# Kernel tuning notes

Hardware: AMD Instinct MI355X
Metric: run time of the kernel (lower is better)

The kernel has to match this reference:

```python
import jax, jax.numpy as jnp
import numpy as np

EPS = 1e-5   # torch BatchNorm2d default eps
HEADS = 4


def conv1x1_bn(x, w, g, b, m, v):
    # 1x1 conv (no bias) == channel matmul, then inference-mode BatchNorm
    y = jnp.einsum('oc,bchw->bohw', w, x)
    s = g / jnp.sqrt(v + EPS)
    return y * s[None, :, None, None] + (b - m * s)[None, :, None, None]


def dwconv3x3_bn(x, w, g, b, m, v):
    # depthwise 3x3 conv, padding 1 (autopad), groups=C, then BatchNorm
    C = x.shape[1]
    y = jax.lax.conv_general_dilated(
        x, w, window_strides=(1, 1), padding=((1, 1), (1, 1)),
        dimension_numbers=('NCHW', 'OIHW', 'NCHW'), feature_group_count=C)
    s = g / jnp.sqrt(v + EPS)
    return y * s[None, :, None, None] + (b - m * s)[None, :, None, None]


def split_heads(x):
    b, c, h, w = x.shape
    hd = c // HEADS
    return x.reshape(b, HEADS, hd, h * w).transpose(0, 1, 3, 2)  # [b,heads,n,hd]


def merge_heads(x, h, w):
    b, heads, n, hd = x.shape
    return x.transpose(0, 1, 3, 2).reshape(b, heads * hd, h, w)


def setup_inputs() -> dict:
    key = jax.random.key(0)
    B, C, H, W = 4, 256, 48, 48
    ks = jax.random.split(key, 32)
    inp = {
        'q': jax.random.normal(ks[0], (B, C, H, W), jnp.float32),
        'k': jax.random.normal(ks[1], (B, C, H, W), jnp.float32),
        'v': jax.random.normal(ks[2], (B, C, H, W), jnp.float32),
    }
    i = 3
    for name in ['wq', 'wk', 'wv', 'proj']:
        inp[name + '_w'] = jax.random.normal(ks[i], (C, C), jnp.float32) * 0.02; i += 1
    inp['pe_w'] = jax.random.normal(ks[i], (C, 1, 3, 3), jnp.float32) * 0.1; i += 1
    for name in ['wq', 'wk', 'wv', 'pe', 'proj']:
        inp[name + '_g'] = jax.random.uniform(ks[i], (C,), jnp.float32, 0.5, 1.5); i += 1
        inp[name + '_b'] = jax.random.normal(ks[i], (C,), jnp.float32) * 0.1; i += 1
        inp[name + '_m'] = jax.random.normal(ks[i], (C,), jnp.float32) * 0.1; i += 1
        inp[name + '_v'] = jax.random.uniform(ks[i], (C,), jnp.float32, 0.5, 1.5); i += 1
    return inp


def reference(q, k, v,
              wq_w, wk_w, wv_w, proj_w, pe_w,
              wq_g, wq_b, wq_m, wq_v,
              wk_g, wk_b, wk_m, wk_v,
              wv_g, wv_b, wv_m, wv_v,
              pe_g, pe_b, pe_m, pe_v,
              proj_g, proj_b, proj_m, proj_v):
    H, W = q.shape[2], q.shape[3]
    qf = conv1x1_bn(q, wq_w, wq_g, wq_b, wq_m, wq_v)
    kf = conv1x1_bn(k, wk_w, wk_g, wk_b, wk_m, wk_v)
    vf = conv1x1_bn(v, wv_w, wv_g, wv_b, wv_m, wv_v)
    qh = split_heads(qf)  # [b,heads,n,hd]
    kh = split_heads(kf)
    vh = split_heads(vf)
    scale = qh.shape[-1] ** -0.5
    attn = jax.nn.softmax(jnp.einsum('bhnd,bhmd->bhnm', qh, kh) * scale, axis=-1)
    y = jnp.einsum('bhnm,bhmd->bhnd', attn, vh)
    y = merge_heads(y, H, W) + dwconv3x3_bn(merge_heads(qh, H, W), pe_w, pe_g, pe_b, pe_m, pe_v)
    return conv1x1_bn(y, proj_w, proj_g, proj_b, proj_m, proj_v)
```

## Files before the change

### kernel.cpp

```cpp
#include <hip/hip_runtime.h>
#include <math.h>

#define HEADS 4
#define HD    64
#define CCH   256
#define NB    4
#define HH    48
#define WW    48
#define NN    (HH*WW)
#define EPSBN 1e-5f
#define KSCL  0.18033688f
#define BCN   (NB*CCH*NN)
#define NSP   4

typedef unsigned short ushort_t;
typedef __attribute__((ext_vector_type(8))) short bfrag;
typedef __attribute__((ext_vector_type(4))) float f32x4;

#define MFMA __builtin_amdgcn_mfma_f32_16x16x32_bf16

static __device__ __forceinline__ ushort_t f2bf(float x) {
    unsigned int u = __float_as_uint(x);
    unsigned int r = (u + 0x7fffu + ((u >> 16) & 1u)) >> 16;
    return (ushort_t)r;
}
static __device__ __forceinline__ unsigned cvtpk(float lo, float hi) {
    unsigned r;
    asm("v_cvt_pk_bf16_f32 %0, %1, %2" : "=v"(r) : "v"(lo), "v"(hi));
    return r;
}
static __device__ __forceinline__ float bflo(unsigned u) { return __uint_as_float(u << 16); }
static __device__ __forceinline__ float bfhi(unsigned u) { return __uint_as_float(u & 0xffff0000u); }

static __device__ __forceinline__ void gload16(const void* g, void* l) {
    __builtin_amdgcn_global_load_lds(
        (const __attribute__((address_space(1))) void*)g,
        (__attribute__((address_space(3))) void*)l, 16, 0, 0);
}

struct PrepWP {
    const float* W[4];
    const float* G[4]; const float* Bb[4]; const float* Mm[4]; const float* Vv[4];
    const float* pew; const float* peg; const float* peb; const float* pem; const float* pev;
    ushort_t* W4; float* bias4; ushort_t* pw2; float* pbias; float* kmax2;
    const float* q; const float* k; const float* v; ushort_t* Xt;
};
__global__ __launch_bounds__(256)
void prep_kernel(PrepWP P)
{
    const int blk = blockIdx.x, tid = threadIdx.x;
    if (blk < 3456) {
        const int t  = blk / 1152;
        const int r  = blk % 1152;
        const int b  = r / 288;
        const int r2 = r % 288;
        const int n0 = (r2 >> 3) * 64;
        const int cb = (r2 & 7) * 32;
        const float* X = (t == 0) ? P.q : (t == 1) ? P.k : P.v;
        ushort_t* O = P.Xt + (size_t)t * BCN;
        const int lane = tid & 63;
        const int c0   = cb + (tid >> 6) * 8;
        const float* src = X + ((size_t)(b * CCH + c0) * NN + n0 + lane);
        float vv[8];
#pragma unroll
        for (int j = 0; j < 8; ++j) vv[j] = src[(size_t)j * NN];
        uint4 u;
        u.x = cvtpk(vv[0], vv[1]); u.y = cvtpk(vv[2], vv[3]);
        u.z = cvtpk(vv[4], vv[5]); u.w = cvtpk(vv[6], vv[7]);
        *(uint4*)&O[((size_t)b * NN + n0 + lane) * CCH + c0] = u;
        return;
    }
    const int wb = blk - 3456;
    if (wb == 128) {
        int c = tid;
        float s = P.peg[c] * rsqrtf(P.pev[c] + EPSBN);
        for (int tap = 0; tap < 9; ++tap)
            P.pw2[tap * CCH + c] = f2bf(P.pew[c * 9 + tap] * s);
        P.pbias[c] = P.peb[c] - P.pem[c] * s;
        if (tid < 16) P.kmax2[tid] = 0.f;
        return;
    }
    int g  = wb * 256 + tid;
    int cv = g >> 13;
    int o  = (g >> 5) & 255;
    int c8 = g & 31;
    float s  = P.G[cv][o] * rsqrtf(P.Vv[cv][o] + EPSBN);
    float s2 = (cv == 1) ? s * KSCL : s;
    const float* w = P.W[cv] + (size_t)o * CCH + c8 * 8;
    uint4 u;
    u.x = cvtpk(w[0]*s2, w[1]*s2); u.y = cvtpk(w[2]*s2, w[3]*s2);
    u.z = cvtpk(w[4]*s2, w[5]*s2); u.w = cvtpk(w[6]*s2, w[7]*s2);
    *(uint4*)&P.W4[((size_t)cv * CCH + o) * CCH + c8 * 8] = u;
    if (c8 == 0) {
        float bb = (P.Bb[cv][o] - P.Mm[cv][o] * s);
        P.bias4[cv * CCH + o] = (cv == 1) ? bb * KSCL : bb;
    }
}

template<int PROJ>
__global__ __launch_bounds__(256)
void conv_gemm(const ushort_t* __restrict__ T, const ushort_t* __restrict__ W4,
               const float* __restrict__ bias4,
               ushort_t* __restrict__ qnd, ushort_t* __restrict__ knd,
               ushort_t* __restrict__ vcn, float* __restrict__ outf,
               float* __restrict__ kmax2)
{
    __shared__ ushort_t Ts[64][264];
    __shared__ ushort_t Ws[64][264];
    const int nt = blockIdx.x, ot = blockIdx.y, z = blockIdx.z;
    const int which = PROJ ? 3 : (z >> 2);
    const int b = z & 3;
    const int tid = threadIdx.x;
    const int n0 = nt * 64, o0 = ot * 64;
    const ushort_t* Tsrc = T + (PROJ ? (size_t)0 : (size_t)which * BCN) + ((size_t)b * NN + n0) * CCH;
    const ushort_t* Wsrc = W4 + (size_t)which * CCH * CCH + (size_t)o0 * CCH;
    const float*    bias = bias4 + which * CCH;
#pragma unroll
    for (int i = 0; i < 8; ++i) {
        int idx = tid + i * 256;
        int r = idx >> 5, c16 = idx & 31;
        *(uint4*)&Ts[r][c16 * 8] = *(const uint4*)&Tsrc[(size_t)r * CCH + c16 * 8];
        *(uint4*)&Ws[r][c16 * 8] = *(const uint4*)&Wsrc[(size_t)r * CCH + c16 * 8];
    }
    __syncthreads();
    const int wv = tid >> 6, lane = tid & 63, lr = lane & 15, lg = lane >> 4;
    const int qn = (wv >> 1) * 32, qo = (wv & 1) * 32;
    f32x4 acc[2][2];
#pragma unroll
    for (int i = 0; i < 2; ++i)
#pragma unroll
        for (int j = 0; j < 2; ++j) acc[i][j] = (f32x4){0.f, 0.f, 0.f, 0.f};

    if (!PROJ && (z >> 2) < 2) {
#pragma unroll
        for (int k8 = 0; k8 < 8; ++k8) {
            const int kc = k8 * 32 + lg * 8;
            bfrag ta0 = *(const bfrag*)&Ts[qn + lr][kc];
            bfrag ta1 = *(const bfrag*)&Ts[qn + 16 + lr][kc];
            bfrag wa0 = *(const bfrag*)&Ws[qo + lr][kc];
            bfrag wa1 = *(const bfrag*)&Ws[qo + 16 + lr][kc];
            acc[0][0] = MFMA(ta0, wa0, acc[0][0], 0, 0, 0);
            acc[0][1] = MFMA(ta0, wa1, acc[0][1], 0, 0, 0);
            acc[1][0] = MFMA(ta1, wa0, acc[1][0], 0, 0, 0);
            acc[1][1] = MFMA(ta1, wa1, acc[1][1], 0, 0, 0);
        }
    } else {
#pragma unroll
        for (int k8 = 0; k8 < 8; ++k8) {
            const int kc = k8 * 32 + lg * 8;
            bfrag ta0 = *(const bfrag*)&Ts[qn + lr][kc];
            bfrag ta1 = *(const bfrag*)&Ts[qn + 16 + lr][kc];
            bfrag wa0 = *(const bfrag*)&Ws[qo + lr][kc];
            bfrag wa1 = *(const bfrag*)&Ws[qo + 16 + lr][kc];
            acc[0][0] = MFMA(wa0, ta0, acc[0][0], 0, 0, 0);
            acc[0][1] = MFMA(wa0, ta1, acc[0][1], 0, 0, 0);
            acc[1][0] = MFMA(wa1, ta0, acc[1][0], 0, 0, 0);
            acc[1][1] = MFMA(wa1, ta1, acc[1][1], 0, 0, 0);
        }
    }

    __syncthreads();
    if (!PROJ && which < 2) {
        ushort_t (*Ot)[72] = (ushort_t(*)[72])Ts;
        float bv[2] = { bias[o0 + qo + lr], bias[o0 + qo + 16 + lr] };
#pragma unroll
        for (int i = 0; i < 2; ++i)
#pragma unroll
            for (int j = 0; j < 2; ++j)
#pragma unroll
                for (int r = 0; r < 4; ++r)
                    Ot[qn + i * 16 + lg * 4 + r][qo + j * 16 + lr] = f2bf(acc[i][j][r] + bv[j]);
        __syncthreads();
        ushort_t* out = (which == 0) ? qnd : knd;
        for (int idx = tid; idx < 512; idx += 256) {
            int r = idx >> 3, sg = idx & 7;
            *(uint4*)&out[(((size_t)b * HEADS + ot) * NN + n0 + r) * HD + sg * 8] =
                *(const uint4*)&Ot[r][sg * 8];
        }
        if (which == 1 && tid < 64) {
            float s = 0.f;
#pragma unroll
            for (int j = 0; j < 8; ++j) {
                uint4 u = *(const uint4*)&Ot[tid][j * 8];
                s += bflo(u.x)*bflo(u.x) + bfhi(u.x)*bfhi(u.x);
                s += bflo(u.y)*bflo(u.y) + bfhi(u.y)*bfhi(u.y);
                s += bflo(u.z)*bflo(u.z) + bfhi(u.z)*bfhi(u.z);
                s += bflo(u.w)*bflo(u.w) + bfhi(u.w)*bfhi(u.w);
            }
            atomicMax((unsigned*)&kmax2[b * HEADS + ot], __float_as_uint(s));
        }
    } else if (!PROJ) {
        ushort_t (*Ot)[72] = (ushort_t(*)[72])Ts;
#pragma unroll
        for (int i = 0; i < 2; ++i)
#pragma unroll
            for (int r = 0; r < 4; ++r) {
                float bv = bias[o0 + qo + i * 16 + lg * 4 + r];
#pragma unroll
                for (int j = 0; j < 2; ++j)
                    Ot[qo + i * 16 + lg * 4 + r][qn + j * 16 + lr] = f2bf(acc[i][j][r] + bv);
            }
        __syncthreads();
        for (int idx = tid; idx < 512; idx += 256) {
            int r = idx >> 3, sg = idx & 7;
            *(uint4*)&vcn[((size_t)b * CCH + o0 + r) * NN + n0 + sg * 8] =
                *(const uint4*)&Ot[r][sg * 8];
        }
    } else {
        float (*Of)[68] = (float(*)[68])Ts;
#pragma unroll
        for (int i = 0; i < 2; ++i)
#pragma unroll
            for (int r = 0; r < 4; ++r) {
                float bv = bias[o0 + qo + i * 16 + lg * 4 + r];
#pragma unroll
                for (int j = 0; j < 2; ++j)
                    Of[qo + i * 16 + lg * 4 + r][qn + j * 16 + lr] = acc[i][j][r] + bv;
            }
        __syncthreads();
        for (int idx = tid; idx < 1024; idx += 256) {
            int r = idx >> 4, c4 = idx & 15;
            *(float4*)&outf[((size_t)b * CCH + o0 + r) * NN + n0 + c4 * 4] =
                *(const float4*)&Of[r][c4 * 4];
        }
    }
}

__global__ __launch_bounds__(256, 4)
void attn_kernel(const ushort_t* __restrict__ Qnd,
                 const ushort_t* __restrict__ Knd,
                 const ushort_t* __restrict__ Vcn,
                 const float* __restrict__ kmax2,
                 ushort_t* __restrict__ Op,
                 float* __restrict__ Larr)
{
    __shared__ __align__(16) char smem[32768];

    const int tid = threadIdx.x;
    const int lin0 = blockIdx.x + 18 * blockIdx.y + 288 * blockIdx.z;
    const int w    = (lin0 & 7) * 144 + (lin0 >> 3);
    const int qt = w % 18;
    const int bh = (w / 18) & 15;
    const int sp = w / 288;
    const int b = bh >> 2, h = bh & 3;
    const int lane = tid & 63, wv = tid >> 6;
    const int lr = lane & 15, lg = lane >> 4;
    const int lrow = lane >> 3, lslot = (lane & 7) ^ lrow;
    const int n0 = qt * 128;
    const size_t ndb = (size_t)(b * HEADS + h) * NN * HD;
    const size_t cnb = ((size_t)b * CCH + h * HD) * NN;

    const char* kgp = (const char*)(Knd + ndb) + (size_t)(sp * 576 + wv * 16 + lrow) * 128 + lslot * 16;
    const char* vgp = (const char*)(Vcn + cnb + sp * 576) + (size_t)(wv * 16 + lrow) * (NN * 2) + lslot * 16;
    char* kls = smem + wv * 2048;
    char* vls = smem + 16384 + wv * 2048;

#define STAGE_K(buf, t) do { \
    const char* kp_ = kgp + (size_t)(t) * 8192; \
    char* kd_ = kls + (buf) * 8192; \
    gload16(kp_,        kd_); \
    gload16(kp_ + 1024, kd_ + 1024); \
} while (0)
#define STAGE_V(buf, t) do { \
    const char* vp_ = vgp + (size_t)(t) * 128; \
    char* vd_ = vls + (buf) * 8192; \
    gload16(vp_,              vd_); \
    gload16(vp_ + 8 * (NN*2), vd_ + 1024); \
} while (0)

    bfrag qb[2][2];
    {
        const ushort_t* qbase = Qnd + ndb + (size_t)(n0 + wv * 32 + lr) * HD;
        qb[0][0] = *(const bfrag*)&qbase[lg * 8];
        qb[0][1] = *(const bfrag*)&qbase[32 + lg * 8];
        qb[1][0] = *(const bfrag*)&qbase[16 * HD + lg * 8];
        qb[1][1] = *(const bfrag*)&qbase[16 * HD + 32 + lg * 8];
    }
    float m0[2];
    {
        const float kmx = sqrtf(kmax2[bh]);
#pragma unroll
        for (int qc = 0; qc < 2; ++qc) {
            const unsigned* u0 = (const unsigned*)&qb[qc][0];
            const unsigned* u1 = (const unsigned*)&qb[qc][1];
            float s = 0.f;
#pragma unroll
            for (int j = 0; j < 4; ++j) {
                float a0 = bflo(u0[j]), a1 = bfhi(u0[j]);
                float b0 = bflo(u1[j]), b1 = bfhi(u1[j]);
                s += a0*a0 + a1*a1 + b0*b0 + b1*b1;
            }
            s += __shfl_xor(s, 16);
            s += __shfl_xor(s, 32);
            m0[qc] = sqrtf(s) * kmx + 0.5f;
        }
    }
    bfrag ones_f;
    {
        short ov = (lr == 0) ? (short)0x3F80 : (short)0;
#pragma unroll
        for (int j = 0; j < 8; ++j) ones_f[j] = ov;
    }

    f32x4 o[2][4], o4[2];
#pragma unroll
    for (int qc = 0; qc < 2; ++qc) {
        o4[qc] = (f32x4){0.f, 0.f, 0.f, 0.f};
#pragma unroll
        for (int db = 0; db < 4; ++db) o[qc][db] = (f32x4){0.f, 0.f, 0.f, 0.f};
    }

    const int sw0 = (lg ^ (lr & 7)) << 4;
    const int sw1 = ((4 + lg) ^ (lr & 7)) << 4;

    STAGE_K(0, 0);
    STAGE_V(0, 0);
    __syncthreads();

    for (int t = 0; t < 9; ++t) {
        const int cur = t & 1;
        if (t < 8) STAGE_K(cur ^ 1, t + 1);
        const char* Kb = smem + cur * 8192;
        const char* Vb = smem + 16384 + cur * 8192;
        char* Pw = smem + 16384 + (cur ^ 1) * 8192 + wv * 2048;

        uint2 pd[2][4];
#pragma unroll
        for (int kb = 0; kb < 4; ++kb) {
            const char* krow = Kb + (kb * 16 + lr) * 128;
            bfrag ka0 = *(const bfrag*)(krow + sw0);
            bfrag ka1 = *(const bfrag*)(krow + sw1);
            f32x4 z0 = (f32x4){-m0[0], -m0[0], -m0[0], -m0[0]};
            z0 = MFMA(ka0, qb[0][0], z0, 0, 0, 0);
            f32x4 s0 = MFMA(ka1, qb[0][1], z0, 0, 0, 0);
            f32x4 z1 = (f32x4){-m0[1], -m0[1], -m0[1], -m0[1]};
            z1 = MFMA(ka0, qb[1][0], z1, 0, 0, 0);
            f32x4 s1 = MFMA(ka1, qb[1][1], z1, 0, 0, 0);
            pd[0][kb].x = cvtpk(exp2f(s0[0]), exp2f(s0[1]));
            pd[0][kb].y = cvtpk(exp2f(s0[2]), exp2f(s0[3]));
            pd[1][kb].x = cvtpk(exp2f(s1[0]), exp2f(s1[1]));
            pd[1][kb].y = cvtpk(exp2f(s1[2]), exp2f(s1[3]));
        }

        bfrag pb[2][2];
#pragma unroll
        for (int qc = 0; qc < 2; ++qc) {
            char* prow = Pw + lr * 128;
#pragma unroll
            for (int kb = 0; kb < 4; ++kb) {
                int slot = (2 * kb + (lg >> 1)) ^ (lr & 7);
                *(uint2*)(prow + slot * 16 + (lg & 1) * 8) = pd[qc][kb];
            }
            pb[qc][0] = *(const bfrag*)(prow + sw0);
            pb[qc][1] = *(const bfrag*)(prow + sw1);
        }
        asm volatile("s_waitcnt lgkmcnt(0)" ::: "memory");
        if (t < 8) STAGE_V(cur ^ 1, t + 1);

#pragma unroll
        for (int db = 0; db < 4; ++db) {
            const char* vrow = Vb + (db * 16 + lr) * 128;
            bfrag va0 = *(const bfrag*)(vrow + sw0);
            bfrag va1 = *(const bfrag*)(vrow + sw1);
            o[0][db] = MFMA(va0, pb[0][0], o[0][db], 0, 0, 0);
            o[0][db] = MFMA(va1, pb[0][1], o[0][db], 0, 0, 0);
            o[1][db] = MFMA(va0, pb[1][0], o[1][db], 0, 0, 0);
            o[1][db] = MFMA(va1, pb[1][1], o[1][db], 0, 0, 0);
        }
        o4[0] = MFMA(ones_f, pb[0][0], o4[0], 0, 0, 0);
        o4[0] = MFMA(ones_f, pb[0][1], o4[0], 0, 0, 0);
        o4[1] = MFMA(ones_f, pb[1][0], o4[1], 0, 0, 0);
        o4[1] = MFMA(ones_f, pb[1][1], o4[1], 0, 0, 0);

        __syncthreads();
    }
#undef STAGE_K
#undef STAGE_V

    if (lg == 0) {
#pragma unroll
        for (int qc = 0; qc < 2; ++qc)
            Larr[(size_t)(sp * 16 + bh) * NN + n0 + wv * 32 + qc * 16 + lr] = o4[qc][0];
    }
    unsigned (*Osb)[36] = (unsigned(*)[36])smem;
#pragma unroll
    for (int qc = 0; qc < 2; ++qc) {
        int row = wv * 32 + qc * 16 + lr;
#pragma unroll
        for (int db = 0; db < 4; ++db) {
            Osb[row][db * 8 + lg * 2 + 0] = cvtpk(o[qc][db][0], o[qc][db][1]);
            Osb[row][db * 8 + lg * 2 + 1] = cvtpk(o[qc][db][2], o[qc][db][3]);
        }
    }
    __syncthreads();
    ushort_t* opb = Op + (size_t)sp * BCN + ((size_t)b * NN + n0) * CCH + h * HD;
    for (int idx = tid; idx < 1024; idx += 256) {
        int n = idx >> 3, s4 = idx & 7;
        *(uint4*)&opb[(size_t)n * CCH + s4 * 8] = *(const uint4*)&Osb[n][s4 * 4];
    }
}

__global__ __launch_bounds__(256)
void fuse_kernel(const ushort_t* __restrict__ Op, const float* __restrict__ Larr,
                 const ushort_t* __restrict__ Qnd,
                 const ushort_t* __restrict__ pw2, const float* __restrict__ pbias,
                 ushort_t* __restrict__ yt)
{
    const int tid = threadIdx.x;
    const int b  = blockIdx.x / 288;
    const int n0 = (blockIdx.x % 288) * 8;
    const int c8 = tid & 31, ns = tid >> 5;
    const int n  = n0 + ns;
    const int h  = c8 >> 3, c0 = c8 * 8;

    const ushort_t* o0p = Op + ((size_t)b * NN + n) * CCH + c0;
    float acc[8] = {0.f, 0.f, 0.f, 0.f, 0.f, 0.f, 0.f, 0.f};
#pragma unroll
    for (int s = 0; s < NSP; ++s) {
        uint4 u = *(const uint4*)&o0p[(size_t)s * BCN];
        acc[0] += bflo(u.x); acc[1] += bfhi(u.x);
        acc[2] += bflo(u.y); acc[3] += bfhi(u.y);
        acc[4] += bflo(u.z); acc[5] += bfhi(u.z);
        acc[6] += bflo(u.w); acc[7] += bfhi(u.w);
    }
    int mi = (b * HEADS + h) * NN + n;
    float ls = 0.f;
#pragma unroll
    for (int s = 0; s < NSP; ++s) ls += Larr[(size_t)s * 16 * NN + mi];
    float rinv = 1.0f / ls;
#pragma unroll
    for (int j = 0; j < 8; ++j) acc[j] *= rinv;

    const int x = n % WW, y = n / WW;
    const ushort_t* qb = Qnd + (size_t)(b * HEADS + h) * NN * HD + (c8 & 7) * 8;
#pragma unroll
    for (int ky = 0; ky < 3; ++ky) {
        int yy = y + ky - 1;
        if (yy < 0 || yy >= HH) continue;
#pragma unroll
        for (int kx = 0; kx < 3; ++kx) {
            int xx = x + kx - 1;
            if (xx < 0 || xx >= WW) continue;
            int np = yy * WW + xx;
            uint4 qv = *(const uint4*)&qb[(size_t)np * HD];
            uint4 w4 = *(const uint4*)&pw2[(ky * 3 + kx) * CCH + c0];
            acc[0] += bflo(qv.x) * bflo(w4.x); acc[1] += bfhi(qv.x) * bfhi(w4.x);
            acc[2] += bflo(qv.y) * bflo(w4.y); acc[3] += bfhi(qv.y) * bfhi(w4.y);
            acc[4] += bflo(qv.z) * bflo(w4.z); acc[5] += bfhi(qv.z) * bfhi(w4.z);
            acc[6] += bflo(qv.w) * bflo(w4.w); acc[7] += bfhi(qv.w) * bfhi(w4.w);
        }
    }
    float4 p0 = *(const float4*)&pbias[c0];
    float4 p1 = *(const float4*)&pbias[c0 + 4];
    acc[0] += p0.x; acc[1] += p0.y; acc[2] += p0.z; acc[3] += p0.w;
    acc[4] += p1.x; acc[5] += p1.y; acc[6] += p1.z; acc[7] += p1.w;
    uint4 u;
    u.x = cvtpk(acc[0], acc[1]); u.y = cvtpk(acc[2], acc[3]);
    u.z = cvtpk(acc[4], acc[5]); u.w = cvtpk(acc[6], acc[7]);
    *(uint4*)&yt[((size_t)b * NN + n) * CCH + c0] = u;
}

extern "C" void kernel_launch(void* const* d_in, const int* in_sizes, int n_in,
                              void* d_out, int out_size, void* d_ws, size_t ws_size,
                              hipStream_t stream) {
    char* ws = (char*)d_ws;
    ushort_t* qnd  = (ushort_t*)(ws + 0);
    ushort_t* knd  = (ushort_t*)(ws + 4718592);
    ushort_t* vcn  = (ushort_t*)(ws + 9437184);
    ushort_t* Xt   = (ushort_t*)(ws + 14155776);
    ushort_t* Op   = (ushort_t*)(ws + 14155776);
    ushort_t* yt   = (ushort_t*)(ws + 4718592);
    float*    Larr = (float*)   (ws + 33030144);
    ushort_t* W4   = (ushort_t*)(ws + 33619968);
    float*    bias4= (float*)   (ws + 34144256);
    ushort_t* pw2  = (ushort_t*)(ws + 34148352);
    float*    pbias= (float*)   (ws + 34152960);
    float*    kmax2= (float*)   (ws + 34156032);

    PrepWP P;
    P.W[0] = (const float*)d_in[3]; P.W[1] = (const float*)d_in[4];
    P.W[2] = (const float*)d_in[5]; P.W[3] = (const float*)d_in[6];
    P.G[0]  = (const float*)d_in[8];  P.Bb[0] = (const float*)d_in[9];
    P.Mm[0] = (const float*)d_in[10]; P.Vv[0] = (const float*)d_in[11];
    P.G[1]  = (const float*)d_in[12]; P.Bb[1] = (const float*)d_in[13];
    P.Mm[1] = (const float*)d_in[14]; P.Vv[1] = (const float*)d_in[15];
    P.G[2]  = (const float*)d_in[16]; P.Bb[2] = (const float*)d_in[17];
    P.Mm[2] = (const float*)d_in[18]; P.Vv[2] = (const float*)d_in[19];
    P.G[3]  = (const float*)d_in[24]; P.Bb[3] = (const float*)d_in[25];
    P.Mm[3] = (const float*)d_in[26]; P.Vv[3] = (const float*)d_in[27];
    P.pew = (const float*)d_in[7];
    P.peg = (const float*)d_in[20]; P.peb = (const float*)d_in[21];
    P.pem = (const float*)d_in[22]; P.pev = (const float*)d_in[23];
    P.W4 = W4; P.bias4 = bias4; P.pw2 = pw2; P.pbias = pbias; P.kmax2 = kmax2;
    P.q = (const float*)d_in[0]; P.k = (const float*)d_in[1];
    P.v = (const float*)d_in[2]; P.Xt = Xt;

    prep_kernel<<<3585, 256, 0, stream>>>(P);

    conv_gemm<0><<<dim3(36, 4, 12), 256, 0, stream>>>(Xt, W4, bias4, qnd, knd, vcn, nullptr, kmax2);

    attn_kernel<<<dim3(18, 16, NSP), 256, 0, stream>>>(qnd, knd, vcn, kmax2, Op, Larr);

    fuse_kernel<<<1152, 256, 0, stream>>>(Op, Larr, qnd, pw2, pbias, yt);

    conv_gemm<1><<<dim3(36, 4, 4), 256, 0, stream>>>(yt, W4, bias4, nullptr, nullptr, nullptr,
                                                     (float*)d_out, nullptr);
}
```

Before: 93.64 us.

## Load K/V MFMA fragments directly from global memory, drop LDS staging

The attention kernel stops double-buffering K and V tiles in shared memory through global_load_lds and instead has each lane read its MFMA fragments straight from global memory, relying on L1/L2 for reuse across the four waves. LDS is now used only for per-wave P tiles, so shared memory shrinks and the per-iteration block barrier is removed. The aim is to cut barrier stalls and LDS traffic and allow more resident blocks. In exchange, each wave re-fetches K/V from cache with no explicit prefetch, which exposes global load latency.

```diff
diff --git a/kernel.cpp b/kernel.cpp
--- a/kernel.cpp
+++ b/kernel.cpp
@@ -31,12 +31,6 @@
 }
 static __device__ __forceinline__ float bflo(unsigned u) { return __uint_as_float(u << 16); }
 static __device__ __forceinline__ float bfhi(unsigned u) { return __uint_as_float(u & 0xffff0000u); }
-
-static __device__ __forceinline__ void gload16(const void* g, void* l) {
-    __builtin_amdgcn_global_load_lds(
-        (const __attribute__((address_space(1))) void*)g,
-        (__attribute__((address_space(3))) void*)l, 16, 0, 0);
-}
 
 struct PrepWP {
     const float* W[4];
@@ -234,7 +228,7 @@
                  ushort_t* __restrict__ Op,
                  float* __restrict__ Larr)
 {
-    __shared__ __align__(16) char smem[32768];
+    __shared__ __align__(16) char smem[18432];
 
     const int tid = threadIdx.x;
     const int lin0 = blockIdx.x + 18 * blockIdx.y + 288 * blockIdx.z;
@@ -245,28 +239,13 @@
     const int b = bh >> 2, h = bh & 3;
     const int lane = tid & 63, wv = tid >> 6;
     const int lr = lane & 15, lg = lane >> 4;
-    const int lrow = lane >> 3, lslot = (lane & 7) ^ lrow;
     const int n0 = qt * 128;
     const size_t ndb = (size_t)(b * HEADS + h) * NN * HD;
     const size_t cnb = ((size_t)b * CCH + h * HD) * NN;
-
-    const char* kgp = (const char*)(Knd + ndb) + (size_t)(sp * 576 + wv * 16 + lrow) * 128 + lslot * 16;
-    const char* vgp = (const char*)(Vcn + cnb + sp * 576) + (size_t)(wv * 16 + lrow) * (NN * 2) + lslot * 16;
-    char* kls = smem + wv * 2048;
-    char* vls = smem + 16384 + wv * 2048;
-
-#define STAGE_K(buf, t) do { \
-    const char* kp_ = kgp + (size_t)(t) * 8192; \
-    char* kd_ = kls + (buf) * 8192; \
-    gload16(kp_,        kd_); \
-    gload16(kp_ + 1024, kd_ + 1024); \
-} while (0)
-#define STAGE_V(buf, t) do { \
-    const char* vp_ = vgp + (size_t)(t) * 128; \
-    char* vd_ = vls + (buf) * 8192; \
-    gload16(vp_,              vd_); \
-    gload16(vp_ + 8 * (NN*2), vd_ + 1024); \
-} while (0)
+    const int kb0 = sp * 576;
+
+    const ushort_t* kp = Knd + ndb + (size_t)(kb0 + lr) * HD + lg * 8;
+    const ushort_t* vp = Vcn + cnb + (size_t)lr * NN + kb0 + lg * 8;
 
     bfrag qb[2][2];
     {
@@ -312,24 +291,16 @@
 
     const int sw0 = (lg ^ (lr & 7)) << 4;
     const int sw1 = ((4 + lg) ^ (lr & 7)) << 4;
-
-    STAGE_K(0, 0);
-    STAGE_V(0, 0);
-    __syncthreads();
+    char* Pw0 = smem + wv * 4096;
+    char* Pw1 = Pw0 + 2048;
 
     for (int t = 0; t < 9; ++t) {
-        const int cur = t & 1;
-        if (t < 8) STAGE_K(cur ^ 1, t + 1);
-        const char* Kb = smem + cur * 8192;
-        const char* Vb = smem + 16384 + cur * 8192;
-        char* Pw = smem + 16384 + (cur ^ 1) * 8192 + wv * 2048;
-
         uint2 pd[2][4];
 #pragma unroll
         for (int kb = 0; kb < 4; ++kb) {
-            const char* krow = Kb + (kb * 16 + lr) * 128;
-            bfrag ka0 = *(const bfrag*)(krow + sw0);
-            bfrag ka1 = *(const bfrag*)(krow + sw1);
+            const ushort_t* kr = kp + (size_t)(t * 64 + kb * 16) * HD;
+            bfrag ka0 = *(const bfrag*)kr;
+            bfrag ka1 = *(const bfrag*)(kr + 32);
             f32x4 z0 = (f32x4){-m0[0], -m0[0], -m0[0], -m0[0]};
             z0 = MFMA(ka0, qb[0][0], z0, 0, 0, 0);
             f32x4 s0 = MFMA(ka1, qb[0][1], z0, 0, 0, 0);
@@ -345,7 +316,7 @@
         bfrag pb[2][2];
 #pragma unroll
         for (int qc = 0; qc < 2; ++qc) {
-            char* prow = Pw + lr * 128;
+            char* prow = ((qc == 0) ? Pw0 : Pw1) + lr * 128;
 #pragma unroll
             for (int kb = 0; kb < 4; ++kb) {
                 int slot = (2 * kb + (lg >> 1)) ^ (lr & 7);
@@ -354,14 +325,12 @@
             pb[qc][0] = *(const bfrag*)(prow + sw0);
             pb[qc][1] = *(const bfrag*)(prow + sw1);
         }
-        asm volatile("s_waitcnt lgkmcnt(0)" ::: "memory");
-        if (t < 8) STAGE_V(cur ^ 1, t + 1);
 
 #pragma unroll
         for (int db = 0; db < 4; ++db) {
-            const char* vrow = Vb + (db * 16 + lr) * 128;
-            bfrag va0 = *(const bfrag*)(vrow + sw0);
-            bfrag va1 = *(const bfrag*)(vrow + sw1);
+            const ushort_t* vr = vp + (size_t)(db * 16) * NN + t * 64;
+            bfrag va0 = *(const bfrag*)vr;
+            bfrag va1 = *(const bfrag*)(vr + 32);
             o[0][db] = MFMA(va0, pb[0][0], o[0][db], 0, 0, 0);
             o[0][db] = MFMA(va1, pb[0][1], o[0][db], 0, 0, 0);
             o[1][db] = MFMA(va0, pb[1][0], o[1][db], 0, 0, 0);
@@ -371,17 +340,14 @@
         o4[0] = MFMA(ones_f, pb[0][1], o4[0], 0, 0, 0);
         o4[1] = MFMA(ones_f, pb[1][0], o4[1], 0, 0, 0);
         o4[1] = MFMA(ones_f, pb[1][1], o4[1], 0, 0, 0);
-
-        __syncthreads();
-    }
-#undef STAGE_K
-#undef STAGE_V
+    }
 
     if (lg == 0) {
 #pragma unroll
         for (int qc = 0; qc < 2; ++qc)
             Larr[(size_t)(sp * 16 + bh) * NN + n0 + wv * 32 + qc * 16 + lr] = o4[qc][0];
     }
+    __syncthreads();
     unsigned (*Osb)[36] = (unsigned(*)[36])smem;
 #pragma unroll
     for (int qc = 0; qc < 2; ++qc) {
```

After: 142.4 us. 1.52x slower.
